# Performance work log

Hardware: AMD Instinct MI355X
Metric: run time of the kernel (lower is better)

Reference implementation:

```python
import jax, jax.numpy as jnp
import numpy as np

HEADS = 4
DIM_HEAD = 32
SCALE = DIM_HEAD ** -0.5


def setup_inputs() -> dict:
    key = jax.random.key(0)
    k1, k2, k3 = jax.random.split(key, 3)
    dim = 128
    hidden = HEADS * DIM_HEAD  # 128
    x = jax.random.normal(k1, (4, dim, 64, 64), dtype=jnp.float32)
    w_qkv = jax.random.normal(k2, (3 * hidden, dim), dtype=jnp.float32) * (dim ** -0.5)
    w_out = jax.random.normal(k3, (dim, hidden), dtype=jnp.float32) * (hidden ** -0.5)
    b_out = jnp.zeros((dim,), dtype=jnp.float32)
    return {"x": x, "w_qkv": w_qkv, "w_out": w_out, "b_out": b_out}


def reference(x, w_qkv, w_out, b_out):
    b, c, h, w = x.shape
    n = h * w
    # 1x1 conv == channel matmul per pixel
    qkv = jnp.einsum('oc,bchw->bohw', w_qkv, x)  # [b, 3*hidden, h, w]
    q, k, v = jnp.split(qkv, 3, axis=1)
    # b (heads d) x y -> b heads d (x y)
    def to_heads(t):
        return t.reshape(b, HEADS, DIM_HEAD, n)
    q = to_heads(q) * SCALE
    k = to_heads(k)
    v = to_heads(v)
    sim = jnp.einsum('bhdi,bhdj->bhij', q, k)          # [b, heads, n, n]
    attn = jax.nn.softmax(sim, axis=-1)
    out = jnp.einsum('bhij,bhdj->bhid', attn, v)        # [b, heads, n, d]
    # b h (x y) d -> b (h d) x y
    out = out.transpose(0, 1, 3, 2).reshape(b, HEADS * DIM_HEAD, h, w)
    out = jnp.einsum('oc,bchw->bohw', w_out, out) + b_out[None, :, None, None]
    return out
```

## Files before the change

kernel.cpp:

```cpp
#include <hip/hip_runtime.h>
#include <math.h>

#define NHEAD 4
#define DHEAD 32
#define NPIX  4096
#define CIN   128

typedef __bf16 bf16_t;
typedef __bf16 bf16x8 __attribute__((ext_vector_type(8)));
typedef __bf16 bf16x4 __attribute__((ext_vector_type(4)));
typedef float  f32x4  __attribute__((ext_vector_type(4)));

constexpr float QSCALE = 0.17677669529663687f * 1.4426950408889634f;

__global__ void __launch_bounds__(256) prep_weights(
    const float* __restrict__ w_qkv, const float* __restrict__ w_out,
    ushort* __restrict__ wqkv_bf, ushort* __restrict__ wout_bf) {
  const int i4 = (blockIdx.x * 256 + threadIdx.x) * 4;
  const float* src;
  ushort* dst;
  float sc = 1.f;
  if (i4 < 49152) {
    src = w_qkv + i4; dst = wqkv_bf + i4;
    if (i4 < 16384) sc = QSCALE;
  } else {
    src = w_out + (i4 - 49152); dst = wout_bf + (i4 - 49152);
  }
  float4 v = *(const float4*)src;
  bf16x4 o = {(bf16_t)(v.x * sc), (bf16_t)(v.y * sc),
              (bf16_t)(v.z * sc), (bf16_t)(v.w * sc)};
  *(bf16x4*)dst = o;
}

__global__ void __launch_bounds__(384) qkv_mfma(
    const float* __restrict__ x, const ushort* __restrict__ wqkv,
    ushort* __restrict__ qb, ushort* __restrict__ kb, ushort* __restrict__ vT) {
  __shared__ ushort Xls[64 * 136];
  const int tid = threadIdx.x, cg = tid >> 6, lane = tid & 63;
  const int n = lane & 15, quad = lane >> 4;
  const int b = blockIdx.y, p0 = blockIdx.x * 64;

  bf16x8 wf[4][4];
#pragma unroll
  for (int t1 = 0; t1 < 4; ++t1)
#pragma unroll
    for (int k = 0; k < 4; ++k)
      wf[t1][k] = *(const bf16x8*)(wqkv +
          (size_t)(cg * 64 + t1 * 16 + n) * CIN + k * 32 + quad * 8);

  if (tid < 256) {
    const int pc = tid & 15;
    const int c0 = (tid >> 4) * 4;
#pragma unroll
    for (int pass = 0; pass < 2; ++pass) {
      const int c = c0 + pass * 64;
      const float* xp = x + ((size_t)b * CIN + c) * NPIX + p0 + pc * 4;
      float4 r0 = *(const float4*)xp;
      float4 r1 = *(const float4*)(xp + NPIX);
      float4 r2 = *(const float4*)(xp + 2 * NPIX);
      float4 r3 = *(const float4*)(xp + 3 * NPIX);
      bf16x4 w0 = {(bf16_t)r0.x, (bf16_t)r1.x, (bf16_t)r2.x, (bf16_t)r3.x};
      bf16x4 w1 = {(bf16_t)r0.y, (bf16_t)r1.y, (bf16_t)r2.y, (bf16_t)r3.y};
      bf16x4 w2 = {(bf16_t)r0.z, (bf16_t)r1.z, (bf16_t)r2.z, (bf16_t)r3.z};
      bf16x4 w3 = {(bf16_t)r0.w, (bf16_t)r1.w, (bf16_t)r2.w, (bf16_t)r3.w};
      *(bf16x4*)&Xls[(pc * 4 + 0) * 136 + c] = w0;
      *(bf16x4*)&Xls[(pc * 4 + 1) * 136 + c] = w1;
      *(bf16x4*)&Xls[(pc * 4 + 2) * 136 + c] = w2;
      *(bf16x4*)&Xls[(pc * 4 + 3) * 136 + c] = w3;
    }
  }
  __syncthreads();

  f32x4 acc[4][4];
#pragma unroll
  for (int i = 0; i < 4; ++i)
#pragma unroll
    for (int j = 0; j < 4; ++j) acc[i][j] = (f32x4){0.f, 0.f, 0.f, 0.f};

  const bool isv = (cg >= 4);
#pragma unroll
  for (int k = 0; k < 4; ++k) {
    bf16x8 xf[4];
#pragma unroll
    for (int pt = 0; pt < 4; ++pt)
      xf[pt] = *(const bf16x8*)&Xls[(pt * 16 + n) * 136 + k * 32 + quad * 8];
    if (!isv) {
#pragma unroll
      for (int wt = 0; wt < 4; ++wt)
#pragma unroll
        for (int pt = 0; pt < 4; ++pt)
          acc[wt][pt] = __builtin_amdgcn_mfma_f32_16x16x32_bf16(
              wf[wt][k], xf[pt], acc[wt][pt], 0, 0, 0);
    } else {
#pragma unroll
      for (int pt = 0; pt < 4; ++pt)
#pragma unroll
        for (int ct = 0; ct < 4; ++ct)
          acc[pt][ct] = __builtin_amdgcn_mfma_f32_16x16x32_bf16(
              xf[pt], wf[ct][k], acc[pt][ct], 0, 0, 0);
    }
  }

  if (!isv) {
    ushort* dst0 = (cg < 2) ? qb : kb;
#pragma unroll
    for (int wt = 0; wt < 4; ++wt) {
      const int ch = (cg & 1) * 64 + wt * 16 + quad * 4;
      const int head = ch >> 5, d = ch & 31;
#pragma unroll
      for (int pt = 0; pt < 4; ++pt) {
        const int p = p0 + pt * 16 + n;
        f32x4 a = acc[wt][pt];
        bf16x4 o = {(bf16_t)a[0], (bf16_t)a[1], (bf16_t)a[2], (bf16_t)a[3]};
        *(bf16x4*)(dst0 + ((size_t)(b * NHEAD + head) * NPIX + p) * DHEAD + d) = o;
      }
    }
  } else {
#pragma unroll
    for (int ct = 0; ct < 4; ++ct) {
      const int ch = (cg & 1) * 64 + ct * 16 + n;
      const int head = ch >> 5, d = ch & 31;
#pragma unroll
      for (int pt = 0; pt < 4; ++pt) {
        const int p = p0 + pt * 16 + quad * 4;
        f32x4 a = acc[pt][ct];
        bf16x4 o = {(bf16_t)a[0], (bf16_t)a[1], (bf16_t)a[2], (bf16_t)a[3]};
        *(bf16x4*)(vT + ((size_t)(b * NHEAD + head) * DHEAD + d) * NPIX + p) = o;
      }
    }
  }
}

__global__ void __launch_bounds__(256, 2) flash_mfma(
    const ushort* __restrict__ qb, const ushort* __restrict__ kbuf,
    const ushort* __restrict__ vTb, float* __restrict__ part) {
  __shared__ ushort Kls[64 * 40];
  __shared__ ushort Vls[32 * 72];
  __shared__ ushort Pls[4][64 * 72];

  const int tid   = threadIdx.x;
  const int wave  = tid >> 6;
  const int lane  = tid & 63;
  const int n     = lane & 15;
  const int quad  = lane >> 4;
  const int js    = blockIdx.y;
  const int bh    = blockIdx.z;
  const int qbase = blockIdx.x * 256 + wave * 64;

  const ushort* kg = kbuf + (size_t)bh * NPIX * DHEAD;
  const ushort* vg = vTb + (size_t)bh * DHEAD * NPIX;

  bf16x8 qf[4];
#pragma unroll
  for (int rp = 0; rp < 4; ++rp)
    qf[rp] = *(const bf16x8*)(qb +
        ((size_t)bh * NPIX + qbase + rp * 16 + n) * DHEAD + quad * 8);

  f32x4 O[4][2];
  float lac[4][4];
#pragma unroll
  for (int rp = 0; rp < 4; ++rp) {
#pragma unroll
    for (int dp = 0; dp < 2; ++dp) O[rp][dp] = (f32x4){0.f, 0.f, 0.f, 0.f};
#pragma unroll
    for (int r = 0; r < 4; ++r) lac[rp][r] = 0.f;
  }

  ushort* Pw = Pls[wave];
  const f32x4 zero = {0.f, 0.f, 0.f, 0.f};

  for (int t = 0; t < 32; ++t) {
    const int j0 = js * 2048 + t * 64;
    __syncthreads();
    {
      const int krow = tid >> 2, kseg = tid & 3;
      *(bf16x8*)&Kls[krow * 40 + kseg * 8] =
          *(const bf16x8*)(kg + (size_t)(j0 + krow) * DHEAD + kseg * 8);
      const int vrow = tid >> 3, vseg = tid & 7;
      *(bf16x8*)&Vls[vrow * 72 + vseg * 8] =
          *(const bf16x8*)(vg + (size_t)vrow * NPIX + j0 + vseg * 8);
    }
    __syncthreads();

    bf16x8 kf[4];
#pragma unroll
    for (int f = 0; f < 4; ++f)
      kf[f] = *(const bf16x8*)&Kls[(4 * n + f) * 40 + quad * 8];

#pragma unroll
    for (int rp = 0; rp < 4; ++rp) {
      f32x4 s[4];
#pragma unroll
      for (int f = 0; f < 4; ++f)
        s[f] = __builtin_amdgcn_mfma_f32_16x16x32_bf16(qf[rp], kf[f], zero, 0, 0, 0);
#pragma unroll
      for (int r = 0; r < 4; ++r) {
        const float p0 = __builtin_amdgcn_exp2f(s[0][r]);
        const float p1 = __builtin_amdgcn_exp2f(s[1][r]);
        const float p2 = __builtin_amdgcn_exp2f(s[2][r]);
        const float p3 = __builtin_amdgcn_exp2f(s[3][r]);
        lac[rp][r] += (p0 + p1) + (p2 + p3);
        bf16x4 pv = {(bf16_t)p0, (bf16_t)p1, (bf16_t)p2, (bf16_t)p3};
        *(bf16x4*)&Pw[(rp * 16 + 4 * quad + r) * 72 + 4 * n] = pv;
      }
    }

    bf16x8 vf[2][2];
#pragma unroll
    for (int kb2 = 0; kb2 < 2; ++kb2)
#pragma unroll
      for (int dp = 0; dp < 2; ++dp)
        vf[kb2][dp] = *(const bf16x8*)&Vls[(dp * 16 + n) * 72 + kb2 * 32 + quad * 8];

#pragma unroll
    for (int rp = 0; rp < 4; ++rp)
#pragma unroll
      for (int kb2 = 0; kb2 < 2; ++kb2) {
        bf16x8 pf = *(const bf16x8*)&Pw[(rp * 16 + n) * 72 + kb2 * 32 + quad * 8];
#pragma unroll
        for (int dp = 0; dp < 2; ++dp)
          O[rp][dp] = __builtin_amdgcn_mfma_f32_16x16x32_bf16(pf, vf[kb2][dp], O[rp][dp], 0, 0, 0);
      }
  }

  float* pb = part + ((size_t)js * 65536 + (size_t)bh * NPIX) * 36;
#pragma unroll
  for (int rp = 0; rp < 4; ++rp)
#pragma unroll
    for (int r = 0; r < 4; ++r) {
      float l = lac[rp][r];
      l += __shfl_xor(l, 1);
      l += __shfl_xor(l, 2);
      l += __shfl_xor(l, 4);
      l += __shfl_xor(l, 8);
      const int query = qbase + rp * 16 + 4 * quad + r;
      if (n == 0) pb[(size_t)query * 36 + 32] = l;
#pragma unroll
      for (int dp = 0; dp < 2; ++dp)
        pb[(size_t)query * 36 + dp * 16 + n] = O[rp][dp][r];
    }
}

__global__ void __launch_bounds__(256) combine2(
    const float* __restrict__ part, ushort* __restrict__ aoT) {
  const int idx = blockIdx.x * 256 + threadIdx.x;
  const float* p0 = part + (size_t)idx * 36;
  const float* p1 = part + (size_t)(65536 + idx) * 36;
  const float inv = 1.f / (p0[32] + p1[32]);
#pragma unroll
  for (int t = 0; t < 4; ++t) {
    float4 a0 = ((const float4*)p0)[2 * t];
    float4 a1 = ((const float4*)p0)[2 * t + 1];
    float4 b0 = ((const float4*)p1)[2 * t];
    float4 b1 = ((const float4*)p1)[2 * t + 1];
    bf16x8 o = {(bf16_t)((a0.x + b0.x) * inv), (bf16_t)((a0.y + b0.y) * inv),
                (bf16_t)((a0.z + b0.z) * inv), (bf16_t)((a0.w + b0.w) * inv),
                (bf16_t)((a1.x + b1.x) * inv), (bf16_t)((a1.y + b1.y) * inv),
                (bf16_t)((a1.z + b1.z) * inv), (bf16_t)((a1.w + b1.w) * inv)};
    *(bf16x8*)(aoT + (size_t)idx * 32 + t * 8) = o;
  }
}

__global__ void __launch_bounds__(256) out_mfma(
    const ushort* __restrict__ aoT, const ushort* __restrict__ wob,
    const float* __restrict__ bias, float* __restrict__ out) {
  const int tid = threadIdx.x, wv = tid >> 6, lane = tid & 63;
  const int n = lane & 15, quad = lane >> 4;
  const int b = blockIdx.y;
  const int p = blockIdx.x * 64 + wv * 16 + n;

  bf16x8 wf[8][4];
#pragma unroll
  for (int mt = 0; mt < 8; ++mt)
#pragma unroll
    for (int k = 0; k < 4; ++k)
      wf[mt][k] = *(const bf16x8*)(wob + (size_t)(mt * 16 + n) * CIN + k * 32 + quad * 8);

  bf16x8 bfr[4];
#pragma unroll
  for (int k = 0; k < 4; ++k)
    bfr[k] = *(const bf16x8*)(aoT + ((size_t)(b * NHEAD + k) * NPIX + p) * DHEAD + quad * 8);

  f32x4 acc[8];
#pragma unroll
  for (int mt = 0; mt < 8; ++mt) acc[mt] = (f32x4){0.f, 0.f, 0.f, 0.f};
#pragma unroll
  for (int k = 0; k < 4; ++k)
#pragma unroll
    for (int mt = 0; mt < 8; ++mt)
      acc[mt] = __builtin_amdgcn_mfma_f32_16x16x32_bf16(wf[mt][k], bfr[k], acc[mt], 0, 0, 0);

#pragma unroll
  for (int mt = 0; mt < 8; ++mt) {
    const int oc = mt * 16 + quad * 4;
#pragma unroll
    for (int r = 0; r < 4; ++r)
      out[((size_t)b * CIN + oc + r) * NPIX + p] = acc[mt][r] + bias[oc + r];
  }
}

extern "C" void kernel_launch(void* const* d_in, const int* in_sizes, int n_in,
                              void* d_out, int out_size, void* d_ws, size_t ws_size,
                              hipStream_t stream) {
  const float* x     = (const float*)d_in[0];
  const float* w_qkv = (const float*)d_in[1];
  const float* w_out = (const float*)d_in[2];
  const float* b_out = (const float*)d_in[3];
  float* out = (float*)d_out;

  char* base = (char*)d_ws;
  ushort* qb      = (ushort*)base;
  ushort* kb      = (ushort*)(base + (size_t)4 * 1024 * 1024);
  ushort* vT      = (ushort*)(base + (size_t)8 * 1024 * 1024);
  ushort* aoT     = (ushort*)(base + (size_t)12 * 1024 * 1024);
  float*  part    = (float*)(base + (size_t)16 * 1024 * 1024);
  ushort* wqkv_bf = (ushort*)(base + (size_t)36 * 1024 * 1024);
  ushort* wout_bf = (ushort*)(base + (size_t)36 * 1024 * 1024 + 128 * 1024);

  prep_weights<<<dim3(64), 256, 0, stream>>>(w_qkv, w_out, wqkv_bf, wout_bf);
  qkv_mfma<<<dim3(64, 4), 384, 0, stream>>>(x, wqkv_bf, qb, kb, vT);
  flash_mfma<<<dim3(16, 2, 16), 256, 0, stream>>>(qb, kb, vT, part);
  combine2<<<dim3(256), 256, 0, stream>>>(part, aoT);
  out_mfma<<<dim3(64, 4), 256, 0, stream>>>(aoT, wout_bf, b_out, out);
}
```

Before: 150.6 us.

## Rework flash attention to register-resident P via transposed MFMA and split-KV by four

```diff
diff --git a/kernel.cpp b/kernel.cpp
--- a/kernel.cpp
+++ b/kernel.cpp
@@ -35,10 +35,10 @@
 __global__ void __launch_bounds__(384) qkv_mfma(
     const float* __restrict__ x, const ushort* __restrict__ wqkv,
     ushort* __restrict__ qb, ushort* __restrict__ kb, ushort* __restrict__ vT) {
-  __shared__ ushort Xls[64 * 136];
+  __shared__ ushort Xls[32 * 136];
   const int tid = threadIdx.x, cg = tid >> 6, lane = tid & 63;
   const int n = lane & 15, quad = lane >> 4;
-  const int b = blockIdx.y, p0 = blockIdx.x * 64;
+  const int b = blockIdx.y, p0 = blockIdx.x * 32;
 
   bf16x8 wf[4][4];
 #pragma unroll
@@ -49,55 +49,51 @@
           (size_t)(cg * 64 + t1 * 16 + n) * CIN + k * 32 + quad * 8);
 
   if (tid < 256) {
-    const int pc = tid & 15;
-    const int c0 = (tid >> 4) * 4;
-#pragma unroll
-    for (int pass = 0; pass < 2; ++pass) {
-      const int c = c0 + pass * 64;
-      const float* xp = x + ((size_t)b * CIN + c) * NPIX + p0 + pc * 4;
-      float4 r0 = *(const float4*)xp;
-      float4 r1 = *(const float4*)(xp + NPIX);
-      float4 r2 = *(const float4*)(xp + 2 * NPIX);
-      float4 r3 = *(const float4*)(xp + 3 * NPIX);
-      bf16x4 w0 = {(bf16_t)r0.x, (bf16_t)r1.x, (bf16_t)r2.x, (bf16_t)r3.x};
-      bf16x4 w1 = {(bf16_t)r0.y, (bf16_t)r1.y, (bf16_t)r2.y, (bf16_t)r3.y};
-      bf16x4 w2 = {(bf16_t)r0.z, (bf16_t)r1.z, (bf16_t)r2.z, (bf16_t)r3.z};
-      bf16x4 w3 = {(bf16_t)r0.w, (bf16_t)r1.w, (bf16_t)r2.w, (bf16_t)r3.w};
-      *(bf16x4*)&Xls[(pc * 4 + 0) * 136 + c] = w0;
-      *(bf16x4*)&Xls[(pc * 4 + 1) * 136 + c] = w1;
-      *(bf16x4*)&Xls[(pc * 4 + 2) * 136 + c] = w2;
-      *(bf16x4*)&Xls[(pc * 4 + 3) * 136 + c] = w3;
-    }
+    const int pc = tid & 7;
+    const int c  = (tid >> 3) * 4;
+    const float* xp = x + ((size_t)b * CIN + c) * NPIX + p0 + pc * 4;
+    float4 r0 = *(const float4*)xp;
+    float4 r1 = *(const float4*)(xp + NPIX);
+    float4 r2 = *(const float4*)(xp + 2 * NPIX);
+    float4 r3 = *(const float4*)(xp + 3 * NPIX);
+    bf16x4 w0 = {(bf16_t)r0.x, (bf16_t)r1.x, (bf16_t)r2.x, (bf16_t)r3.x};
+    bf16x4 w1 = {(bf16_t)r0.y, (bf16_t)r1.y, (bf16_t)r2.y, (bf16_t)r3.y};
+    bf16x4 w2 = {(bf16_t)r0.z, (bf16_t)r1.z, (bf16_t)r2.z, (bf16_t)r3.z};
+    bf16x4 w3 = {(bf16_t)r0.w, (bf16_t)r1.w, (bf16_t)r2.w, (bf16_t)r3.w};
+    *(bf16x4*)&Xls[(pc * 4 + 0) * 136 + c] = w0;
+    *(bf16x4*)&Xls[(pc * 4 + 1) * 136 + c] = w1;
+    *(bf16x4*)&Xls[(pc * 4 + 2) * 136 + c] = w2;
+    *(bf16x4*)&Xls[(pc * 4 + 3) * 136 + c] = w3;
   }
   __syncthreads();
 
-  f32x4 acc[4][4];
+  f32x4 acc[4][2];
 #pragma unroll
   for (int i = 0; i < 4; ++i)
 #pragma unroll
-    for (int j = 0; j < 4; ++j) acc[i][j] = (f32x4){0.f, 0.f, 0.f, 0.f};
+    for (int j = 0; j < 2; ++j) acc[i][j] = (f32x4){0.f, 0.f, 0.f, 0.f};
 
   const bool isv = (cg >= 4);
 #pragma unroll
   for (int k = 0; k < 4; ++k) {
-    bf16x8 xf[4];
-#pragma unroll
-    for (int pt = 0; pt < 4; ++pt)
+    bf16x8 xf[2];
+#pragma unroll
+    for (int pt = 0; pt < 2; ++pt)
       xf[pt] = *(const bf16x8*)&Xls[(pt * 16 + n) * 136 + k * 32 + quad * 8];
     if (!isv) {
 #pragma unroll
       for (int wt = 0; wt < 4; ++wt)
 #pragma unroll
-        for (int pt = 0; pt < 4; ++pt)
+        for (int pt = 0; pt < 2; ++pt)
           acc[wt][pt] = __builtin_amdgcn_mfma_f32_16x16x32_bf16(
               wf[wt][k], xf[pt], acc[wt][pt], 0, 0, 0);
     } else {
 #pragma unroll
-      for (int pt = 0; pt < 4; ++pt)
-#pragma unroll
-        for (int ct = 0; ct < 4; ++ct)
-          acc[pt][ct] = __builtin_amdgcn_mfma_f32_16x16x32_bf16(
-              xf[pt], wf[ct][k], acc[pt][ct], 0, 0, 0);
+      for (int ct = 0; ct < 4; ++ct)
+#pragma unroll
+        for (int pt = 0; pt < 2; ++pt)
+          acc[ct][pt] = __builtin_amdgcn_mfma_f32_16x16x32_bf16(
+              xf[pt], wf[ct][k], acc[ct][pt], 0, 0, 0);
     }
   }
 
@@ -108,7 +104,7 @@
       const int ch = (cg & 1) * 64 + wt * 16 + quad * 4;
       const int head = ch >> 5, d = ch & 31;
 #pragma unroll
-      for (int pt = 0; pt < 4; ++pt) {
+      for (int pt = 0; pt < 2; ++pt) {
         const int p = p0 + pt * 16 + n;
         f32x4 a = acc[wt][pt];
         bf16x4 o = {(bf16_t)a[0], (bf16_t)a[1], (bf16_t)a[2], (bf16_t)a[3]};
@@ -121,9 +117,9 @@
       const int ch = (cg & 1) * 64 + ct * 16 + n;
       const int head = ch >> 5, d = ch & 31;
 #pragma unroll
-      for (int pt = 0; pt < 4; ++pt) {
+      for (int pt = 0; pt < 2; ++pt) {
         const int p = p0 + pt * 16 + quad * 4;
-        f32x4 a = acc[pt][ct];
+        f32x4 a = acc[ct][pt];
         bf16x4 o = {(bf16_t)a[0], (bf16_t)a[1], (bf16_t)a[2], (bf16_t)a[3]};
         *(bf16x4*)(vT + ((size_t)(b * NHEAD + head) * DHEAD + d) * NPIX + p) = o;
       }
@@ -131,168 +127,154 @@
   }
 }
 
+__device__ __forceinline__ void ft_load(const ushort* kb0, const ushort* vb0,
+                                        int t, bf16x8* kf, bf16x8* vf) {
+#pragma unroll
+  for (int p = 0; p < 2; ++p) {
+#pragma unroll
+    for (int s = 0; s < 2; ++s)
+      kf[p * 2 + s] = *(const bf16x8*)(kb0 + (size_t)(t * 64 + p * 32 + s * 4) * DHEAD);
+#pragma unroll
+    for (int dp = 0; dp < 2; ++dp)
+      vf[p * 2 + dp] = *(const bf16x8*)(vb0 + (size_t)dp * 16 * NPIX + t * 64 + p * 32);
+  }
+}
+
+__device__ __forceinline__ void ft_compute(const bf16x8* qf, const bf16x8* kf,
+                                           const bf16x8* vf, const bf16x8 ones,
+                                           f32x4 O[8][2], f32x4* Ol) {
+  const f32x4 zero = {0.f, 0.f, 0.f, 0.f};
+#pragma unroll
+  for (int p = 0; p < 2; ++p) {
+#pragma unroll
+    for (int rp = 0; rp < 8; ++rp) {
+      f32x4 sa = __builtin_amdgcn_mfma_f32_16x16x32_bf16(kf[p * 2 + 0], qf[rp], zero, 0, 0, 0);
+      f32x4 sb = __builtin_amdgcn_mfma_f32_16x16x32_bf16(kf[p * 2 + 1], qf[rp], zero, 0, 0, 0);
+      bf16x8 pf;
+#pragma unroll
+      for (int r = 0; r < 4; ++r) {
+        pf[r]     = (bf16_t)__builtin_amdgcn_exp2f(sa[r]);
+        pf[r + 4] = (bf16_t)__builtin_amdgcn_exp2f(sb[r]);
+      }
+      O[rp][0] = __builtin_amdgcn_mfma_f32_16x16x32_bf16(pf, vf[p * 2 + 0], O[rp][0], 0, 0, 0);
+      O[rp][1] = __builtin_amdgcn_mfma_f32_16x16x32_bf16(pf, vf[p * 2 + 1], O[rp][1], 0, 0, 0);
+      Ol[rp]   = __builtin_amdgcn_mfma_f32_16x16x32_bf16(pf, ones, Ol[rp], 0, 0, 0);
+    }
+  }
+}
+
 __global__ void __launch_bounds__(256, 2) flash_mfma(
     const ushort* __restrict__ qb, const ushort* __restrict__ kbuf,
     const ushort* __restrict__ vTb, float* __restrict__ part) {
-  __shared__ ushort Kls[64 * 40];
-  __shared__ ushort Vls[32 * 72];
-  __shared__ ushort Pls[4][64 * 72];
-
-  const int tid   = threadIdx.x;
-  const int wave  = tid >> 6;
-  const int lane  = tid & 63;
-  const int n     = lane & 15;
-  const int quad  = lane >> 4;
-  const int js    = blockIdx.y;
-  const int bh    = blockIdx.z;
-  const int qbase = blockIdx.x * 256 + wave * 64;
+  const int tid = threadIdx.x, wave = tid >> 6, lane = tid & 63;
+  const int n = lane & 15, quad = lane >> 4;
+  const int js = blockIdx.y, bh = blockIdx.z;
+  const int qrel = blockIdx.x * 512 + wave * 128;
 
   const ushort* kg = kbuf + (size_t)bh * NPIX * DHEAD;
   const ushort* vg = vTb + (size_t)bh * DHEAD * NPIX;
 
-  bf16x8 qf[4];
-#pragma unroll
-  for (int rp = 0; rp < 4; ++rp)
+  bf16x8 qf[8];
+#pragma unroll
+  for (int rp = 0; rp < 8; ++rp)
     qf[rp] = *(const bf16x8*)(qb +
-        ((size_t)bh * NPIX + qbase + rp * 16 + n) * DHEAD + quad * 8);
-
-  f32x4 O[4][2];
-  float lac[4][4];
-#pragma unroll
-  for (int rp = 0; rp < 4; ++rp) {
-#pragma unroll
-    for (int dp = 0; dp < 2; ++dp) O[rp][dp] = (f32x4){0.f, 0.f, 0.f, 0.f};
-#pragma unroll
-    for (int r = 0; r < 4; ++r) lac[rp][r] = 0.f;
-  }
-
-  ushort* Pw = Pls[wave];
-  const f32x4 zero = {0.f, 0.f, 0.f, 0.f};
-
-  for (int t = 0; t < 32; ++t) {
-    const int j0 = js * 2048 + t * 64;
-    __syncthreads();
-    {
-      const int krow = tid >> 2, kseg = tid & 3;
-      *(bf16x8*)&Kls[krow * 40 + kseg * 8] =
-          *(const bf16x8*)(kg + (size_t)(j0 + krow) * DHEAD + kseg * 8);
-      const int vrow = tid >> 3, vseg = tid & 7;
-      *(bf16x8*)&Vls[vrow * 72 + vseg * 8] =
-          *(const bf16x8*)(vg + (size_t)vrow * NPIX + j0 + vseg * 8);
-    }
-    __syncthreads();
-
-    bf16x8 kf[4];
-#pragma unroll
-    for (int f = 0; f < 4; ++f)
-      kf[f] = *(const bf16x8*)&Kls[(4 * n + f) * 40 + quad * 8];
-
-#pragma unroll
-    for (int rp = 0; rp < 4; ++rp) {
-      f32x4 s[4];
-#pragma unroll
-      for (int f = 0; f < 4; ++f)
-        s[f] = __builtin_amdgcn_mfma_f32_16x16x32_bf16(qf[rp], kf[f], zero, 0, 0, 0);
-#pragma unroll
-      for (int r = 0; r < 4; ++r) {
-        const float p0 = __builtin_amdgcn_exp2f(s[0][r]);
-        const float p1 = __builtin_amdgcn_exp2f(s[1][r]);
-        const float p2 = __builtin_amdgcn_exp2f(s[2][r]);
-        const float p3 = __builtin_amdgcn_exp2f(s[3][r]);
-        lac[rp][r] += (p0 + p1) + (p2 + p3);
-        bf16x4 pv = {(bf16_t)p0, (bf16_t)p1, (bf16_t)p2, (bf16_t)p3};
-        *(bf16x4*)&Pw[(rp * 16 + 4 * quad + r) * 72 + 4 * n] = pv;
-      }
-    }
-
-    bf16x8 vf[2][2];
-#pragma unroll
-    for (int kb2 = 0; kb2 < 2; ++kb2)
-#pragma unroll
-      for (int dp = 0; dp < 2; ++dp)
-        vf[kb2][dp] = *(const bf16x8*)&Vls[(dp * 16 + n) * 72 + kb2 * 32 + quad * 8];
-
-#pragma unroll
-    for (int rp = 0; rp < 4; ++rp)
-#pragma unroll
-      for (int kb2 = 0; kb2 < 2; ++kb2) {
-        bf16x8 pf = *(const bf16x8*)&Pw[(rp * 16 + n) * 72 + kb2 * 32 + quad * 8];
-#pragma unroll
-        for (int dp = 0; dp < 2; ++dp)
-          O[rp][dp] = __builtin_amdgcn_mfma_f32_16x16x32_bf16(pf, vf[kb2][dp], O[rp][dp], 0, 0, 0);
-      }
-  }
-
-  float* pb = part + ((size_t)js * 65536 + (size_t)bh * NPIX) * 36;
-#pragma unroll
-  for (int rp = 0; rp < 4; ++rp)
+        ((size_t)bh * NPIX + qrel + rp * 16 + n) * DHEAD + quad * 8);
+
+  f32x4 O[8][2], Ol[8];
+#pragma unroll
+  for (int rp = 0; rp < 8; ++rp) {
+    O[rp][0] = (f32x4){0.f, 0.f, 0.f, 0.f};
+    O[rp][1] = (f32x4){0.f, 0.f, 0.f, 0.f};
+    Ol[rp]   = (f32x4){0.f, 0.f, 0.f, 0.f};
+  }
+  const bf16_t one = (bf16_t)1.0f;
+  const bf16x8 ones = {one, one, one, one, one, one, one, one};
+
+  const int pk = ((n >> 2) << 3) | (n & 3);
+  const ushort* kb0 = kg + (size_t)(js * 1024 + pk) * DHEAD + quad * 8;
+  const ushort* vb0 = vg + (size_t)n * NPIX + js * 1024 + quad * 8;
+
+  bf16x8 kA[4], vA[4], kB[4], vB[4];
+  ft_load(kb0, vb0, 0, kA, vA);
+#pragma unroll 1
+  for (int t = 0; t < 16; t += 2) {
+    ft_load(kb0, vb0, t + 1, kB, vB);
+    ft_compute(qf, kA, vA, ones, O, Ol);
+    if (t + 2 < 16) ft_load(kb0, vb0, t + 2, kA, vA);
+    ft_compute(qf, kB, vB, ones, O, Ol);
+  }
+
+  float* pb = part + ((size_t)js * 65536 + (size_t)bh * NPIX + qrel) * 36;
+#pragma unroll
+  for (int rp = 0; rp < 8; ++rp)
 #pragma unroll
     for (int r = 0; r < 4; ++r) {
-      float l = lac[rp][r];
-      l += __shfl_xor(l, 1);
-      l += __shfl_xor(l, 2);
-      l += __shfl_xor(l, 4);
-      l += __shfl_xor(l, 8);
-      const int query = qbase + rp * 16 + 4 * quad + r;
-      if (n == 0) pb[(size_t)query * 36 + 32] = l;
-#pragma unroll
-      for (int dp = 0; dp < 2; ++dp)
-        pb[(size_t)query * 36 + dp * 16 + n] = O[rp][dp][r];
-    }
-}
-
-__global__ void __launch_bounds__(256) combine2(
+      const int q = rp * 16 + quad * 4 + r;
+      pb[(size_t)q * 36 + n]      = O[rp][0][r];
+      pb[(size_t)q * 36 + 16 + n] = O[rp][1][r];
+      if (n == 0) pb[(size_t)q * 36 + 32] = Ol[rp][r];
+    }
+}
+
+__global__ void __launch_bounds__(256) combine4(
     const float* __restrict__ part, ushort* __restrict__ aoT) {
   const int idx = blockIdx.x * 256 + threadIdx.x;
   const float* p0 = part + (size_t)idx * 36;
-  const float* p1 = part + (size_t)(65536 + idx) * 36;
-  const float inv = 1.f / (p0[32] + p1[32]);
+  const float* p1 = p0 + (size_t)65536 * 36;
+  const float* p2 = p1 + (size_t)65536 * 36;
+  const float* p3 = p2 + (size_t)65536 * 36;
+  const float inv = 1.f / (p0[32] + p1[32] + p2[32] + p3[32]);
 #pragma unroll
   for (int t = 0; t < 4; ++t) {
-    float4 a0 = ((const float4*)p0)[2 * t];
-    float4 a1 = ((const float4*)p0)[2 * t + 1];
-    float4 b0 = ((const float4*)p1)[2 * t];
-    float4 b1 = ((const float4*)p1)[2 * t + 1];
-    bf16x8 o = {(bf16_t)((a0.x + b0.x) * inv), (bf16_t)((a0.y + b0.y) * inv),
-                (bf16_t)((a0.z + b0.z) * inv), (bf16_t)((a0.w + b0.w) * inv),
-                (bf16_t)((a1.x + b1.x) * inv), (bf16_t)((a1.y + b1.y) * inv),
-                (bf16_t)((a1.z + b1.z) * inv), (bf16_t)((a1.w + b1.w) * inv)};
+    float4 a0 = ((const float4*)p0)[2 * t], a1 = ((const float4*)p0)[2 * t + 1];
+    float4 b0 = ((const float4*)p1)[2 * t], b1 = ((const float4*)p1)[2 * t + 1];
+    float4 c0 = ((const float4*)p2)[2 * t], c1 = ((const float4*)p2)[2 * t + 1];
+    float4 d0 = ((const float4*)p3)[2 * t], d1 = ((const float4*)p3)[2 * t + 1];
+    bf16x8 o = {(bf16_t)((a0.x + b0.x + c0.x + d0.x) * inv),
+                (bf16_t)((a0.y + b0.y + c0.y + d0.y) * inv),
+                (bf16_t)((a0.z + b0.z + c0.z + d0.z) * inv),
+                (bf16_t)((a0.w + b0.w + c0.w + d0.w) * inv),
+                (bf16_t)((a1.x + b1.x + c1.x + d1.x) * inv),
+                (bf16_t)((a1.y + b1.y + c1.y + d1.y) * inv),
+                (bf16_t)((a1.z + b1.z + c1.z + d1.z) * inv),
+                (bf16_t)((a1.w + b1.w + c1.w + d1.w) * inv)};
     *(bf16x8*)(aoT + (size_t)idx * 32 + t * 8) = o;
   }
 }
 
-__global__ void __launch_bounds__(256) out_mfma(
+__global__ void __launch_bounds__(512) out_mfma(
     const ushort* __restrict__ aoT, const ushort* __restrict__ wob,
     const float* __restrict__ bias, float* __restrict__ out) {
   const int tid = threadIdx.x, wv = tid >> 6, lane = tid & 63;
   const int n = lane & 15, quad = lane >> 4;
   const int b = blockIdx.y;
-  const int p = blockIdx.x * 64 + wv * 16 + n;
-
-  bf16x8 wf[8][4];
-#pragma unroll
-  for (int mt = 0; mt < 8; ++mt)
+  const int oc0 = (wv & 1) * 64;
+  const int p = blockIdx.x * 64 + (wv >> 1) * 16 + n;
+
+  bf16x8 wf[4][4];
+#pragma unroll
+  for (int mt = 0; mt < 4; ++mt)
 #pragma unroll
     for (int k = 0; k < 4; ++k)
-      wf[mt][k] = *(const bf16x8*)(wob + (size_t)(mt * 16 + n) * CIN + k * 32 + quad * 8);
+      wf[mt][k] = *(const bf16x8*)(wob + (size_t)(oc0 + mt * 16 + n) * CIN + k * 32 + quad * 8);
 
   bf16x8 bfr[4];
 #pragma unroll
   for (int k = 0; k < 4; ++k)
     bfr[k] = *(const bf16x8*)(aoT + ((size_t)(b * NHEAD + k) * NPIX + p) * DHEAD + quad * 8);
 
-  f32x4 acc[8];
-#pragma unroll
-  for (int mt = 0; mt < 8; ++mt) acc[mt] = (f32x4){0.f, 0.f, 0.f, 0.f};
+  f32x4 acc[4];
+#pragma unroll
+  for (int mt = 0; mt < 4; ++mt) acc[mt] = (f32x4){0.f, 0.f, 0.f, 0.f};
 #pragma unroll
   for (int k = 0; k < 4; ++k)
 #pragma unroll
-    for (int mt = 0; mt < 8; ++mt)
+    for (int mt = 0; mt < 4; ++mt)
       acc[mt] = __builtin_amdgcn_mfma_f32_16x16x32_bf16(wf[mt][k], bfr[k], acc[mt], 0, 0, 0);
 
 #pragma unroll
-  for (int mt = 0; mt < 8; ++mt) {
-    const int oc = mt * 16 + quad * 4;
+  for (int mt = 0; mt < 4; ++mt) {
+    const int oc = oc0 + mt * 16 + quad * 4;
 #pragma unroll
     for (int r = 0; r < 4; ++r)
       out[((size_t)b * CIN + oc + r) * NPIX + p] = acc[mt][r] + bias[oc + r];
@@ -313,13 +295,13 @@
   ushort* kb      = (ushort*)(base + (size_t)4 * 1024 * 1024);
   ushort* vT      = (ushort*)(base + (size_t)8 * 1024 * 1024);
   ushort* aoT     = (ushort*)(base + (size_t)12 * 1024 * 1024);
-  float*  part    = (float*)(base + (size_t)16 * 1024 * 1024);
-  ushort* wqkv_bf = (ushort*)(base + (size_t)36 * 1024 * 1024);
-  ushort* wout_bf = (ushort*)(base + (size_t)36 * 1024 * 1024 + 128 * 1024);
+  ushort* wqkv_bf = (ushort*)(base + (size_t)16 * 1024 * 1024);
+  ushort* wout_bf = (ushort*)(base + (size_t)16 * 1024 * 1024 + 96 * 1024);
+  float*  part    = (float*)(base + (size_t)17 * 1024 * 1024);
 
   prep_weights<<<dim3(64), 256, 0, stream>>>(w_qkv, w_out, wqkv_bf, wout_bf);
-  qkv_mfma<<<dim3(64, 4), 384, 0, stream>>>(x, wqkv_bf, qb, kb, vT);
-  flash_mfma<<<dim3(16, 2, 16), 256, 0, stream>>>(qb, kb, vT, part);
-  combine2<<<dim3(256), 256, 0, stream>>>(part, aoT);
-  out_mfma<<<dim3(64, 4), 256, 0, stream>>>(aoT, wout_bf, b_out, out);
-}
+  qkv_mfma<<<dim3(128, 4), 384, 0, stream>>>(x, wqkv_bf, qb, kb, vT);
+  flash_mfma<<<dim3(8, 4, 16), 256, 0, stream>>>(qb, kb, vT, part);
+  combine4<<<dim3(256), 256, 0, stream>>>(part, aoT);
+  out_mfma<<<dim3(64, 4), 512, 0, stream>>>(aoT, wout_bf, b_out, out);
+}
```

New measurement: 140.4 us. 1.07x faster.
